# Optimization experiments

Measured on AMD Instinct MI355X. Metric: run time of the kernel, lower is better.

The kernel has to match this reference:

```python
import jax, jax.numpy as jnp
import numpy as np

MAX_DISP = 4  # max_displacement; window = (2*MAX_DISP+1)**2 = 81 displacements


def setup_inputs() -> dict:
    key = jax.random.key(0)
    k1, k2 = jax.random.split(key)
    B, C, H, W = 8, 128, 128, 128
    in1 = jax.random.normal(k1, (B, C, H, W), dtype=jnp.float32)
    in2 = jax.random.normal(k2, (B, C, H, W), dtype=jnp.float32)
    return {"in1": in1, "in2": in2}


def reference(in1, in2):
    # Cost-volume correlation (kernel_size=1): for each displacement (dy,dx) in
    # [-d, d]^2, corr[b, w, y, x] = mean_c in1[b,c,y,x] * in2_pad[b,c,y+dy,x+dx],
    # matching torch unfold ordering: w = dy_idx*(2d+1) + dx_idx (row-major).
    B, C, H, W = in1.shape
    d = MAX_DISP
    in2_pad = jnp.pad(in2, ((0, 0), (0, 0), (d, d), (d, d)))  # zero pad, like ConstantPad2d
    corr = [
        jnp.mean(in1 * jax.lax.slice(in2_pad, (0, 0, dy, dx), (B, C, dy + H, dx + W)), axis=1)
        for dy in range(2 * d + 1)
        for dx in range(2 * d + 1)
    ]
    return jnp.stack(corr, axis=1)  # [B, (2d+1)^2, H, W]
```

## Files before the change

### kernel.cpp

```cpp
#include <hip/hip_runtime.h>


#define MAXD 4
#define ND 9
#define NDISP 81
#define BATCH 8
#define CH 128
#define HH 128
#define WW 128
#define CC 8
#define NCHUNK (CH / CC)
#define TY 4
#define NROW (TY + 2 * MAXD)
#define P2 136
#define NT 576

__global__ __launch_bounds__(NT) void corr_kernel(
    const float* __restrict__ in1,
    const float* __restrict__ in2,
    float* __restrict__ out)
{
    __shared__ float s2[NROW * CC * P2];

    const int tid = threadIdx.x;
    const int b  = blockIdx.x;
    const int y0 = blockIdx.y * TY;

    for (int j = tid; j < NROW * CC * 8; j += NT) {
        int row = j / (CC * 8);
        int rem = j - row * (CC * 8);
        int c  = rem >> 3;
        int pp = rem & 7;
        int p  = (pp < 4) ? pp : (WW + pp);
        s2[(row * CC + c) * P2 + p] = 0.0f;
    }
    for (int row = 0; row < NROW; ++row) {
        int r = y0 + row - MAXD;
        if (r < 0 || r >= HH) {
            for (int j = tid; j < CC * WW; j += NT) {
                int c = j >> 7;
                int x = j & 127;
                s2[(row * CC + c) * P2 + 4 + x] = 0.0f;
            }
        }
    }

    const int ly = tid / (ND * 16);
    const int dy = (tid / 16) % ND;
    const int xg = tid & 15;
    const int x0 = xg * 4;
    const int rl = ly + dy;

    float acc0[ND][4], acc1[ND][4];
    #pragma unroll
    for (int d = 0; d < ND; ++d)
        #pragma unroll
        for (int i = 0; i < 4; ++i) { acc0[d][i] = 0.0f; acc1[d][i] = 0.0f; }

    const float* in2b   = in2 + (size_t)b * CH * HH * WW;
    const float* in1row = in1 + (size_t)b * CH * HH * WW + (size_t)(y0 + ly) * WW;

    for (int ch = 0; ch < NCHUNK; ++ch) {
        const int c0 = ch * CC;
        __syncthreads();

        for (int j = tid; j < NROW * CC * 32; j += NT) {
            int row = j >> 8;
            int c   = (j >> 5) & 7;
            int xq  = j & 31;
            int r   = y0 + row - MAXD;
            if (r >= 0 && r < HH) {
                float4 v = *(const float4*)(in2b + ((size_t)(c0 + c) * HH + r) * WW + xq * 4);
                *(float4*)&s2[(row * CC + c) * P2 + 4 + xq * 4] = v;
            }
        }
        __syncthreads();

        #pragma unroll
        for (int c = 0; c < CC; ++c) {
            const float* s2r = &s2[(rl * CC + c) * P2];
            float4 b0a = *(const float4*)(s2r + x0);
            float4 b0b = *(const float4*)(s2r + x0 + 4);
            float4 b0c = *(const float4*)(s2r + x0 + 8);
            float4 b1a = *(const float4*)(s2r + x0 + 64);
            float4 b1b = *(const float4*)(s2r + x0 + 68);
            float4 b1c = *(const float4*)(s2r + x0 + 72);
            float bb0[12] = {b0a.x, b0a.y, b0a.z, b0a.w,
                             b0b.x, b0b.y, b0b.z, b0b.w,
                             b0c.x, b0c.y, b0c.z, b0c.w};
            float bb1[12] = {b1a.x, b1a.y, b1a.z, b1a.w,
                             b1b.x, b1b.y, b1b.z, b1b.w,
                             b1c.x, b1c.y, b1c.z, b1c.w};

            const float* p1 = in1row + (size_t)(c0 + c) * HH * WW;
            float4 a0 = *(const float4*)(p1 + x0);
            float4 a1 = *(const float4*)(p1 + x0 + 64);
            float aa0[4] = {a0.x, a0.y, a0.z, a0.w};
            float aa1[4] = {a1.x, a1.y, a1.z, a1.w};

            #pragma unroll
            for (int d = 0; d < ND; ++d) {
                #pragma unroll
                for (int i = 0; i < 4; ++i) {
                    acc0[d][i] = fmaf(aa0[i], bb0[i + d], acc0[d][i]);
                    acc1[d][i] = fmaf(aa1[i], bb1[i + d], acc1[d][i]);
                }
            }
        }
    }

    const float scale = 1.0f / (float)CH;
    float* outb = out + (size_t)b * NDISP * HH * WW + (size_t)(y0 + ly) * WW;
    #pragma unroll
    for (int d = 0; d < ND; ++d) {
        float* op = outb + (size_t)(dy * ND + d) * HH * WW;
        float4 v0 = make_float4(acc0[d][0] * scale, acc0[d][1] * scale,
                                acc0[d][2] * scale, acc0[d][3] * scale);
        float4 v1 = make_float4(acc1[d][0] * scale, acc1[d][1] * scale,
                                acc1[d][2] * scale, acc1[d][3] * scale);
        *(float4*)(op + x0)      = v0;
        *(float4*)(op + x0 + 64) = v1;
    }
}

extern "C" void kernel_launch(void* const* d_in, const int* in_sizes, int n_in,
                              void* d_out, int out_size, void* d_ws, size_t ws_size,
                              hipStream_t stream) {
    const float* in1 = (const float*)d_in[0];
    const float* in2 = (const float*)d_in[1];
    float* out = (float*)d_out;
    dim3 grid(BATCH, HH / TY);
    corr_kernel<<<grid, NT, 0, stream>>>(in1, in2, out);
}
```

Before: 226.1 us.

## Split width into two tiles per block and halve per-thread accumulators

Adds a third grid dimension so each block handles a 64-column tile instead of the full 128-column row. Each thread now keeps 36 accumulators instead of 72, and a launch-bound hint of 5 blocks per CU is added to raise occupancy. The staged in2 tile carries its halo columns, and zero padding is written directly during the load, replacing the separate zeroing pass. The grid doubles in size, and in2 halo rows and columns are reloaded by neighbouring blocks, which adds redundant global traffic.

```diff
diff --git a/kernel.cpp b/kernel.cpp
--- a/kernel.cpp
+++ b/kernel.cpp
@@ -12,38 +12,22 @@
 #define NCHUNK (CH / CC)
 #define TY 4
 #define NROW (TY + 2 * MAXD)
-#define P2 136
+#define XW 64
+#define P2 72
 #define NT 576
+#define NQ 18
 
-__global__ __launch_bounds__(NT) void corr_kernel(
+__global__ __launch_bounds__(NT, 5) void corr_kernel(
     const float* __restrict__ in1,
     const float* __restrict__ in2,
     float* __restrict__ out)
 {
     __shared__ float s2[NROW * CC * P2];
 
-    const int tid = threadIdx.x;
-    const int b  = blockIdx.x;
-    const int y0 = blockIdx.y * TY;
-
-    for (int j = tid; j < NROW * CC * 8; j += NT) {
-        int row = j / (CC * 8);
-        int rem = j - row * (CC * 8);
-        int c  = rem >> 3;
-        int pp = rem & 7;
-        int p  = (pp < 4) ? pp : (WW + pp);
-        s2[(row * CC + c) * P2 + p] = 0.0f;
-    }
-    for (int row = 0; row < NROW; ++row) {
-        int r = y0 + row - MAXD;
-        if (r < 0 || r >= HH) {
-            for (int j = tid; j < CC * WW; j += NT) {
-                int c = j >> 7;
-                int x = j & 127;
-                s2[(row * CC + c) * P2 + 4 + x] = 0.0f;
-            }
-        }
-    }
+    const int tid   = threadIdx.x;
+    const int b     = blockIdx.x;
+    const int y0    = blockIdx.y * TY;
+    const int xbase = blockIdx.z * XW;
 
     const int ly = tid / (ND * 16);
     const int dy = (tid / 16) % ND;
@@ -51,75 +35,67 @@
     const int x0 = xg * 4;
     const int rl = ly + dy;
 
-    float acc0[ND][4], acc1[ND][4];
+    float acc[ND][4];
     #pragma unroll
     for (int d = 0; d < ND; ++d)
         #pragma unroll
-        for (int i = 0; i < 4; ++i) { acc0[d][i] = 0.0f; acc1[d][i] = 0.0f; }
+        for (int i = 0; i < 4; ++i) acc[d][i] = 0.0f;
 
     const float* in2b   = in2 + (size_t)b * CH * HH * WW;
-    const float* in1row = in1 + (size_t)b * CH * HH * WW + (size_t)(y0 + ly) * WW;
+    const float* in1row = in1 + (size_t)b * CH * HH * WW
+                              + (size_t)(y0 + ly) * WW + xbase;
 
     for (int ch = 0; ch < NCHUNK; ++ch) {
         const int c0 = ch * CC;
         __syncthreads();
 
-        for (int j = tid; j < NROW * CC * 32; j += NT) {
-            int row = j >> 8;
-            int c   = (j >> 5) & 7;
-            int xq  = j & 31;
+        #pragma unroll
+        for (int jj = 0; jj < 3; ++jj) {
+            int j   = tid + jj * NT;
+            int row = j / (CC * NQ);
+            int rem = j - row * (CC * NQ);
+            int c   = rem / NQ;
+            int q   = rem - c * NQ;
             int r   = y0 + row - MAXD;
-            if (r >= 0 && r < HH) {
-                float4 v = *(const float4*)(in2b + ((size_t)(c0 + c) * HH + r) * WW + xq * 4);
-                *(float4*)&s2[(row * CC + c) * P2 + 4 + xq * 4] = v;
-            }
+            int gx  = xbase - MAXD + q * 4;
+            float4 v = make_float4(0.0f, 0.0f, 0.0f, 0.0f);
+            if (r >= 0 && r < HH && gx >= 0 && gx + 3 < WW)
+                v = *(const float4*)(in2b + ((size_t)(c0 + c) * HH + r) * WW + gx);
+            *(float4*)&s2[(row * CC + c) * P2 + q * 4] = v;
         }
         __syncthreads();
 
         #pragma unroll
         for (int c = 0; c < CC; ++c) {
-            const float* s2r = &s2[(rl * CC + c) * P2];
-            float4 b0a = *(const float4*)(s2r + x0);
-            float4 b0b = *(const float4*)(s2r + x0 + 4);
-            float4 b0c = *(const float4*)(s2r + x0 + 8);
-            float4 b1a = *(const float4*)(s2r + x0 + 64);
-            float4 b1b = *(const float4*)(s2r + x0 + 68);
-            float4 b1c = *(const float4*)(s2r + x0 + 72);
-            float bb0[12] = {b0a.x, b0a.y, b0a.z, b0a.w,
-                             b0b.x, b0b.y, b0b.z, b0b.w,
-                             b0c.x, b0c.y, b0c.z, b0c.w};
-            float bb1[12] = {b1a.x, b1a.y, b1a.z, b1a.w,
-                             b1b.x, b1b.y, b1b.z, b1b.w,
-                             b1c.x, b1c.y, b1c.z, b1c.w};
+            const float* p1 = in1row + (size_t)(c0 + c) * HH * WW;
+            float4 a = *(const float4*)(p1 + x0);
+            float aa[4] = {a.x, a.y, a.z, a.w};
 
-            const float* p1 = in1row + (size_t)(c0 + c) * HH * WW;
-            float4 a0 = *(const float4*)(p1 + x0);
-            float4 a1 = *(const float4*)(p1 + x0 + 64);
-            float aa0[4] = {a0.x, a0.y, a0.z, a0.w};
-            float aa1[4] = {a1.x, a1.y, a1.z, a1.w};
+            const float* s2r = &s2[(rl * CC + c) * P2 + x0];
+            float4 b0 = *(const float4*)(s2r);
+            float4 b1 = *(const float4*)(s2r + 4);
+            float4 b2 = *(const float4*)(s2r + 8);
+            float bb[12] = {b0.x, b0.y, b0.z, b0.w,
+                            b1.x, b1.y, b1.z, b1.w,
+                            b2.x, b2.y, b2.z, b2.w};
 
             #pragma unroll
-            for (int d = 0; d < ND; ++d) {
+            for (int d = 0; d < ND; ++d)
                 #pragma unroll
-                for (int i = 0; i < 4; ++i) {
-                    acc0[d][i] = fmaf(aa0[i], bb0[i + d], acc0[d][i]);
-                    acc1[d][i] = fmaf(aa1[i], bb1[i + d], acc1[d][i]);
-                }
-            }
+                for (int i = 0; i < 4; ++i)
+                    acc[d][i] = fmaf(aa[i], bb[i + d], acc[d][i]);
         }
     }
 
     const float scale = 1.0f / (float)CH;
-    float* outb = out + (size_t)b * NDISP * HH * WW + (size_t)(y0 + ly) * WW;
+    float* outb = out + (size_t)b * NDISP * HH * WW
+                      + (size_t)(y0 + ly) * WW + xbase;
     #pragma unroll
     for (int d = 0; d < ND; ++d) {
         float* op = outb + (size_t)(dy * ND + d) * HH * WW;
-        float4 v0 = make_float4(acc0[d][0] * scale, acc0[d][1] * scale,
-                                acc0[d][2] * scale, acc0[d][3] * scale);
-        float4 v1 = make_float4(acc1[d][0] * scale, acc1[d][1] * scale,
-                                acc1[d][2] * scale, acc1[d][3] * scale);
-        *(float4*)(op + x0)      = v0;
-        *(float4*)(op + x0 + 64) = v1;
+        float4 v = make_float4(acc[d][0] * scale, acc[d][1] * scale,
+                               acc[d][2] * scale, acc[d][3] * scale);
+        *(float4*)(op + x0) = v;
     }
 }
 
@@ -129,6 +105,6 @@
     const float* in1 = (const float*)d_in[0];
     const float* in2 = (const float*)d_in[1];
     float* out = (float*)d_out;
-    dim3 grid(BATCH, HH / TY);
+    dim3 grid(BATCH, HH / TY, WW / XW);
     corr_kernel<<<grid, NT, 0, stream>>>(in1, in2, out);
 }
```

After: 232.1 us. +2.6%, slower.
